# Performance work log

Measured on AMD Instinct MI355X. Metric: run time of the kernel, lower is better.

## Reference

```python
import jax, jax.numpy as jnp
import numpy as np

EPS = 1e-8       # slot-attention eps
LN_EPS = 1e-5    # torch LayerNorm default
ITERS = 3        # num_iterations


def _ln(x, g, b):
    m = jnp.mean(x, axis=-1, keepdims=True)
    v = jnp.var(x, axis=-1, keepdims=True)
    return (x - m) * jax.lax.rsqrt(v + LN_EPS) * g + b


def setup_inputs() -> dict:
    key = jax.random.key(0)
    ks = jax.random.split(key, 16)
    B, N, S, D = 64, 4096, 8, 256
    s = 1.0 / np.sqrt(D)
    inp = {}
    inp["inputs"] = jax.random.normal(ks[0], (B, N, D), jnp.float32)
    inp["init_slots"] = jax.random.normal(ks[1], (B, S, D), jnp.float32)
    inp["wq"] = jax.random.normal(ks[2], (D, D), jnp.float32) * s
    inp["bq"] = jnp.zeros((D,), jnp.float32)
    inp["wk"] = jax.random.normal(ks[3], (D, D), jnp.float32) * s
    inp["bk"] = jnp.zeros((D,), jnp.float32)
    inp["wv"] = jax.random.normal(ks[4], (D, D), jnp.float32) * s
    inp["bv"] = jnp.zeros((D,), jnp.float32)
    inp["w_ih"] = jax.random.normal(ks[5], (3 * D, D), jnp.float32) * s
    inp["b_ih"] = jnp.zeros((3 * D,), jnp.float32)
    inp["w_hh"] = jax.random.normal(ks[6], (3 * D, D), jnp.float32) * s
    inp["b_hh"] = jnp.zeros((3 * D,), jnp.float32)
    inp["w1"] = jax.random.normal(ks[7], (D, D), jnp.float32) * s  # fc1_slot (hidden_dim == D)
    inp["b1"] = jnp.zeros((D,), jnp.float32)
    inp["w2"] = jax.random.normal(ks[8], (D, D), jnp.float32) * s  # fc2_slot
    inp["b2"] = jnp.zeros((D,), jnp.float32)
    inp["g_in"] = jnp.ones((D,), jnp.float32)
    inp["b_in"] = jnp.zeros((D,), jnp.float32)
    inp["g_slots"] = jnp.ones((D,), jnp.float32)
    inp["b_slots"] = jnp.zeros((D,), jnp.float32)
    inp["g_ff"] = jnp.ones((D,), jnp.float32)
    inp["b_ff"] = jnp.zeros((D,), jnp.float32)
    return inp


def reference(inputs, init_slots, wq, bq, wk, bk, wv, bv, w_ih, b_ih, w_hh, b_hh,
              w1, b1, w2, b2, g_in, b_in, g_slots, b_slots, g_ff, b_ff):
    D = inputs.shape[-1]
    scale = D ** (-0.5)
    # img_k_v: LayerNorm inputs, project to k, v
    x = _ln(inputs, g_in, b_in)
    k = x @ wk.T + bk  # [B,N,D]
    v = x @ wv.T + bv  # [B,N,D]
    slots = init_slots  # [B,S,D]
    for _ in range(ITERS):
        prev = slots
        sn = _ln(slots, g_slots, b_slots)
        q = sn @ wq.T + bq                                   # [B,S,D]
        dots = jnp.einsum('bid,bjd->bij', q, k) * scale      # [B,S,N]
        attn = jax.nn.softmax(dots, axis=1) + EPS            # softmax over slots
        attn = attn / jnp.sum(attn, axis=-1, keepdims=True)  # normalize over inputs
        updates = jnp.einsum('bjd,bij->bid', v, attn)        # [B,S,D]
        # GRUCell(updates, prev): torch gate ordering r, z, n
        gx = updates @ w_ih.T + b_ih
        gh = prev @ w_hh.T + b_hh
        xr, xz, xn = jnp.split(gx, 3, axis=-1)
        hr, hz, hn = jnp.split(gh, 3, axis=-1)
        r = jax.nn.sigmoid(xr + hr)
        z = jax.nn.sigmoid(xz + hz)
        n = jnp.tanh(xn + r * hn)
        slots = (1.0 - z) * n + z * prev
        # residual MLP
        h = jax.nn.relu(_ln(slots, g_ff, b_ff) @ w1.T + b1)
        slots = slots + h @ w2.T + b2
    return slots
```

## Files before the change

### kernel.cpp

```cpp
#include <hip/hip_runtime.h>
#include <hip/hip_bf16.h>
#include <stdint.h>

typedef unsigned short u16;
typedef __attribute__((ext_vector_type(8))) short short8;
typedef __attribute__((ext_vector_type(4))) float f32x4;

#define NB 64
#define NN 4096
#define NS 8
#define ND 256
#define NSEG 16
#define GROWS (NB*NN)

__device__ inline u16 f2bf(float f) {
    uint32_t u = __float_as_uint(f);
    u = (u + 0x7FFFu + ((u >> 16) & 1u)) >> 16;
    return (u16)u;
}
__device__ inline float bf2f(u16 h) {
    return __uint_as_float(((uint32_t)h) << 16);
}
__device__ inline f32x4 mfma16(short8 a, short8 b, f32x4 c) {
    return __builtin_amdgcn_mfma_f32_16x16x32_bf16(a, b, c, 0, 0, 0);
}

__global__ __launch_bounds__(256) void prep_w(
        const float* __restrict__ wv, const float* __restrict__ wk, const float* __restrict__ wq,
        const float* __restrict__ wih, const float* __restrict__ whh,
        const float* __restrict__ w1, const float* __restrict__ w2,
        u16* __restrict__ wvb, u16* __restrict__ wkTb, u16* __restrict__ wqTb,
        u16* __restrict__ wihb, u16* __restrict__ whhb,
        u16* __restrict__ w1b, u16* __restrict__ w2b) {
    int i = blockIdx.x * 256 + threadIdx.x;
    if (i < 65536) { wvb[i] = f2bf(wv[i]); return; }
    i -= 65536;
    if (i < 65536) { wkTb[i] = f2bf(wk[(i & 255)*256 + (i >> 8)]); return; }
    i -= 65536;
    if (i < 65536) { wqTb[i] = f2bf(wq[(i & 255)*256 + (i >> 8)]); return; }
    i -= 65536;
    if (i < 196608) { wihb[i] = f2bf(wih[i]); return; }
    i -= 196608;
    if (i < 196608) { whhb[i] = f2bf(whh[i]); return; }
    i -= 196608;
    if (i < 65536) { w1b[i] = f2bf(w1[i]); return; }
    i -= 65536;
    if (i < 65536) w2b[i] = f2bf(w2[i]);
}

__global__ __launch_bounds__(256) void prep_M(
        const u16* __restrict__ wkTb, const u16* __restrict__ wqTb, u16* __restrict__ Mb,
        const float* __restrict__ wq, const float* __restrict__ bk, float* __restrict__ uvec) {
    if (blockIdx.x == 16) {
        int m = threadIdx.x;
        float acc = 0.f;
        for (int o = 0; o < 256; o++) acc += wq[o*256 + m] * bk[o];
        uvec[m] = acc;
        return;
    }
    const int d0 = blockIdx.x * 16;
    const int tid = threadIdx.x, wid = tid >> 6, lane = tid & 63;
    const int l15 = lane & 15, quad = lane >> 4, kq = quad * 8;
    short8 af[8];
#pragma unroll
    for (int k = 0; k < 8; k++)
        af[k] = *reinterpret_cast<const short8*>(&wkTb[(size_t)(d0 + l15)*256 + k*32 + kq]);
#pragma unroll
    for (int ct = 0; ct < 4; ct++) {
        int m0 = (wid*4 + ct)*16;
        f32x4 a = (f32x4){0.f,0.f,0.f,0.f};
#pragma unroll
        for (int k = 0; k < 8; k++) {
            short8 bw = *reinterpret_cast<const short8*>(&wqTb[(size_t)(m0 + l15)*256 + k*32 + kq]);
            a = mfma16(af[k], bw, a);
        }
#pragma unroll
        for (int r = 0; r < 4; r++)
            Mb[(size_t)(d0 + quad*4 + r)*256 + m0 + l15] = f2bf(a[r]);
    }
}

__global__ __launch_bounds__(256) void ln_cast(
        const float* __restrict__ inp, const float* __restrict__ g,
        const float* __restrict__ bt, u16* __restrict__ xb, u16* __restrict__ xT) {
    __shared__ u16 xs[64*268];
    const int tid = threadIdx.x, wid = tid >> 6, lane = tid & 63;
    const long r0 = (long)blockIdx.x * 64;
    const int rb = wid * 16;
    float4 g4 = reinterpret_cast<const float4*>(g)[lane];
    float4 b4 = reinterpret_cast<const float4*>(bt)[lane];
#pragma unroll 4
    for (int i = 0; i < 16; i++) {
        int row = rb + i;
        float4 v = reinterpret_cast<const float4*>(inp + (r0 + row)*256)[lane];
        float s = v.x + v.y + v.z + v.w;
        float ss = v.x*v.x + v.y*v.y + v.z*v.z + v.w*v.w;
#pragma unroll
        for (int off = 32; off >= 1; off >>= 1) { s += __shfl_xor(s, off, 64); ss += __shfl_xor(ss, off, 64); }
        float mean = s * (1.0f/256.0f);
        float rstd = rsqrtf(ss * (1.0f/256.0f) - mean*mean + 1e-5f);
        ushort4 o;
        o.x = f2bf((v.x-mean)*rstd*g4.x + b4.x);
        o.y = f2bf((v.y-mean)*rstd*g4.y + b4.y);
        o.z = f2bf((v.z-mean)*rstd*g4.z + b4.z);
        o.w = f2bf((v.w-mean)*rstd*g4.w + b4.w);
        reinterpret_cast<ushort4*>(xb + (r0 + row)*256)[lane] = o;
        int colb = (lane*4) ^ (((row >> 3) & 7) << 4);
        *reinterpret_cast<ushort4*>(&xs[row*268 + colb]) = o;
    }
    __syncthreads();
    const long bb = r0 >> 12, nb0 = r0 & 4095;
#pragma unroll
    for (int pass = 0; pass < 8; pass++) {
        const int d = pass*32 + wid*8 + (lane >> 3);
        const int nc = (lane & 7) * 8;
        const int colr = d ^ ((lane & 7) << 4);
        short8 val;
#pragma unroll
        for (int s2 = 0; s2 < 8; s2++)
            val[s2] = (short)xs[(nc + s2)*268 + colr];
        *reinterpret_cast<short8*>(&xT[((size_t)bb*256 + d)*4096 + nb0 + nc]) = val;
    }
}

__global__ __launch_bounds__(256) void q_proj(
        const float* __restrict__ slots, const u16* __restrict__ Mb,
        const float* __restrict__ uvec,
        const float* __restrict__ gs, const float* __restrict__ bs,
        u16* __restrict__ qb, float* __restrict__ cvec) {
    __shared__ u16 sn[16*264];
    const int b = blockIdx.x;
    const int tid = threadIdx.x, wid = tid >> 6, lane = tid & 63;
    const int l15 = lane & 15, kq = (lane >> 4) * 8;
    for (int rr = wid; rr < 8; rr += 4) {
        float4 v = reinterpret_cast<const float4*>(slots + (size_t)(b*8 + rr)*256)[lane];
        float s = v.x + v.y + v.z + v.w;
        float ss = v.x*v.x + v.y*v.y + v.z*v.z + v.w*v.w;
#pragma unroll
        for (int off = 32; off >= 1; off >>= 1) { s += __shfl_xor(s, off, 64); ss += __shfl_xor(ss, off, 64); }
        float mean = s * (1.f/256.f);
        float rstd = rsqrtf(ss * (1.f/256.f) - mean*mean + 1e-5f);
        float4 g4 = reinterpret_cast<const float4*>(gs)[lane];
        float4 b4 = reinterpret_cast<const float4*>(bs)[lane];
        ushort4 o;
        o.x = f2bf((v.x-mean)*rstd*g4.x + b4.x);
        o.y = f2bf((v.y-mean)*rstd*g4.y + b4.y);
        o.z = f2bf((v.z-mean)*rstd*g4.z + b4.z);
        o.w = f2bf((v.w-mean)*rstd*g4.w + b4.w);
        *reinterpret_cast<ushort4*>(&sn[rr*264 + lane*4]) = o;
    }
    {
        ushort4 z = {0,0,0,0};
        for (int rr = 8 + wid; rr < 16; rr += 4)
            *reinterpret_cast<ushort4*>(&sn[rr*264 + lane*4]) = z;
    }
    __syncthreads();
    {
        int s = tid >> 5, l = tid & 31;
        float p = 0.f;
#pragma unroll
        for (int i = 0; i < 8; i++)
            p += bf2f(sn[s*264 + l*8 + i]) * uvec[l*8 + i];
#pragma unroll
        for (int off = 16; off >= 1; off >>= 1) p += __shfl_xor(p, off, 64);
        if (l == 0) cvec[b*8 + s] = p;
    }
    short8 af[8];
#pragma unroll
    for (int k = 0; k < 8; k++) af[k] = *reinterpret_cast<const short8*>(&sn[l15*264 + k*32 + kq]);
#pragma unroll
    for (int ct = 0; ct < 4; ct++) {
        int o0 = (wid*4 + ct)*16;
        f32x4 a = (f32x4){0.f,0.f,0.f,0.f};
#pragma unroll
        for (int k = 0; k < 8; k++) {
            short8 bw = *reinterpret_cast<const short8*>(&Mb[(size_t)(o0 + l15)*256 + k*32 + kq]);
            a = mfma16(af[k], bw, a);
        }
        if (lane < 32) {
            int sb = (lane >> 4)*4;
#pragma unroll
            for (int r = 0; r < 4; r++)
                qb[(size_t)(b*8 + sb + r)*256 + o0 + l15] = f2bf(a[r]);
        }
    }
}

__global__ __launch_bounds__(256) void attn(
        const u16* __restrict__ qt, const u16* __restrict__ xrow,
        const u16* __restrict__ xcol, const float* __restrict__ cvec,
        float* __restrict__ num_part, float* __restrict__ den_part) {
    __shared__ u16 pb_all[4][16*72];
    __shared__ float red[4][8][260];
    __shared__ float redd[4][8];
    const int b = blockIdx.x >> 4;
    const int seg = blockIdx.x & 15;
    const int tid = threadIdx.x, wid = tid >> 6, lane = tid & 63;
    const int l15 = lane & 15, quad = lane >> 4, kq = quad * 8;
    u16* pb = pb_all[wid];
    {
        short8 z = {0,0,0,0,0,0,0,0};
        int r8 = 8 + (lane >> 3), c8 = (lane & 7)*8;
        *reinterpret_cast<short8*>(&pb[r8*72 + c8]) = z;
    }
    short8 aq[8];
    {
        const u16* qrow = &qt[((size_t)b*8 + (l15 & 7))*256 + kq];
        short8 z = {0,0,0,0,0,0,0,0};
#pragma unroll
        for (int kk = 0; kk < 8; kk++) {
            short8 t = *reinterpret_cast<const short8*>(&qrow[kk*32]);
            aq[kk] = (l15 < 8) ? t : z;
        }
    }
    float cc[4];
#pragma unroll
    for (int r = 0; r < 4; r++) {
        int rowi = quad*4 + r;
        cc[r] = (rowi < 8) ? cvec[b*8 + rowi] : 0.f;
    }
    const int n_w = seg*256 + wid*64;
    const u16* kbase = &xrow[((size_t)b*4096 + n_w + l15)*256 + kq];
    const u16* vbase = &xcol[((size_t)b*256 + l15)*4096 + n_w + kq];
    f32x4 acc[16];
#pragma unroll
    for (int dt = 0; dt < 16; dt++) acc[dt] = (f32x4){0.f,0.f,0.f,0.f};
    float psum[4] = {0.f,0.f,0.f,0.f};
    short8 kf[8];
#pragma unroll
    for (int kk = 0; kk < 8; kk++) kf[kk] = *reinterpret_cast<const short8*>(&kbase[kk*32]);

    f32x4 dots[4];
#pragma unroll
    for (int nt = 0; nt < 4; nt++) {
        short8 kn[8];
        if (nt < 3) {
            const u16* kp = kbase + (size_t)((nt+1)*16)*256;
#pragma unroll
            for (int kk = 0; kk < 8; kk++) kn[kk] = *reinterpret_cast<const short8*>(&kp[kk*32]);
        }
        f32x4 d = (f32x4){0.f,0.f,0.f,0.f};
#pragma unroll
        for (int kk = 0; kk < 8; kk++) d = mfma16(aq[kk], kf[kk], d);
        dots[nt] = d;
        if (nt < 3) {
#pragma unroll
            for (int kk = 0; kk < 8; kk++) kf[kk] = kn[kk];
        }
    }
    short8 v0[2], v1[2];
    {
        v0[0] = *reinterpret_cast<const short8*>(vbase);
        v1[0] = *reinterpret_cast<const short8*>(vbase + 32);
        const u16* vr2 = vbase + (size_t)16*4096;
        v0[1] = *reinterpret_cast<const short8*>(vr2);
        v1[1] = *reinterpret_cast<const short8*>(vr2 + 32);
    }
#pragma unroll
    for (int nt = 0; nt < 4; nt++) {
        float t0 = (dots[nt][0] + cc[0])*0.0625f, t1 = (dots[nt][1] + cc[1])*0.0625f;
        float t2 = (dots[nt][2] + cc[2])*0.0625f, t3 = (dots[nt][3] + cc[3])*0.0625f;
        float m4 = fmaxf(fmaxf(t0,t1), fmaxf(t2,t3));
        float m8 = fmaxf(m4, __shfl_xor(m4, 16, 64));
        float e0 = __expf(t0-m8), e1 = __expf(t1-m8), e2 = __expf(t2-m8), e3 = __expf(t3-m8);
        float s4 = e0+e1+e2+e3;
        float s8 = s4 + __shfl_xor(s4, 16, 64);
        float inv = 1.0f / s8;
        u16 h0 = f2bf(e0*inv + 1e-8f);
        u16 h1 = f2bf(e1*inv + 1e-8f);
        u16 h2 = f2bf(e2*inv + 1e-8f);
        u16 h3 = f2bf(e3*inv + 1e-8f);
        if (lane < 32) {
            int sb = quad*4, col = nt*16 + l15;
            pb[(sb+0)*72 + col] = h0;
            pb[(sb+1)*72 + col] = h1;
            pb[(sb+2)*72 + col] = h2;
            pb[(sb+3)*72 + col] = h3;
            psum[0] += bf2f(h0); psum[1] += bf2f(h1);
            psum[2] += bf2f(h2); psum[3] += bf2f(h3);
        }
    }
    __builtin_amdgcn_s_waitcnt(0xC07F);
    short8 ap0 = *reinterpret_cast<const short8*>(&pb[l15*72 + kq]);
    short8 ap1 = *reinterpret_cast<const short8*>(&pb[l15*72 + 32 + kq]);
#pragma unroll
    for (int dt = 0; dt < 16; dt++) {
        short8 nv0, nv1;
        if (dt < 14) {
            const u16* vn = vbase + (size_t)((dt+2)*16)*4096;
            nv0 = *reinterpret_cast<const short8*>(vn);
            nv1 = *reinterpret_cast<const short8*>(vn + 32);
        }
        acc[dt] = mfma16(ap0, v0[dt&1], acc[dt]);
        acc[dt] = mfma16(ap1, v1[dt&1], acc[dt]);
        if (dt < 14) { v0[dt&1] = nv0; v1[dt&1] = nv1; }
    }
#pragma unroll
    for (int off = 1; off < 16; off <<= 1) {
#pragma unroll
        for (int r = 0; r < 4; r++) psum[r] += __shfl_xor(psum[r], off, 64);
    }
    if (lane < 32) {
        int sb = quad*4;
#pragma unroll
        for (int dt = 0; dt < 16; dt++) {
            int d0 = dt*16 + l15;
#pragma unroll
            for (int r = 0; r < 4; r++)
                red[wid][sb+r][d0] = acc[dt][r];
        }
        if (l15 == 0) {
#pragma unroll
            for (int r = 0; r < 4; r++) redd[wid][sb+r] = psum[r];
        }
    }
    __syncthreads();
    for (int idx = tid; idx < 2048; idx += 256) {
        int s = idx >> 8, d = idx & 255;
        float v = red[0][s][d] + red[1][s][d] + red[2][s][d] + red[3][s][d];
        num_part[((size_t)(b*16 + seg)*8 + s)*256 + d] = v;
    }
    if (tid < 8)
        den_part[(b*16 + seg)*8 + tid] = redd[0][tid] + redd[1][tid] + redd[2][tid] + redd[3][tid];
}

__global__ __launch_bounds__(768) void finalize(
        const float* __restrict__ slots_in, const float* __restrict__ num_part, const float* __restrict__ den_part,
        const u16* __restrict__ wihb, const float* __restrict__ bih,
        const u16* __restrict__ whhb, const float* __restrict__ bhh,
        const u16* __restrict__ w1b, const float* __restrict__ b1v,
        const u16* __restrict__ w2b, const float* __restrict__ b2v,
        const u16* __restrict__ wvb, const float* __restrict__ bvv,
        const float* __restrict__ gff, const float* __restrict__ bff,
        float* __restrict__ slots_out,
        const u16* __restrict__ Mb, const float* __restrict__ uvec,
        const float* __restrict__ gs, const float* __restrict__ bs,
        u16* __restrict__ qb, float* __restrict__ cvec, int do_q) {
    __shared__ u16 updb[16*264];
    __shared__ u16 prevb[16*264];
    __shared__ u16 lnb[16*264];
    __shared__ float gx[8*776];
    __shared__ float gh[8*776];
    __shared__ float snew[8*256];
    __shared__ float dsum_s[8];
    float* sfin = gx;
    const int b = blockIdx.x;
    const int tid = threadIdx.x, wid = tid >> 6, lane = tid & 63;
    const int l15 = lane & 15, kq = (lane >> 4) * 8;
    if (tid < 8) {
        float ds = 0.f;
#pragma unroll
        for (int sg = 0; sg < 16; sg++) ds += den_part[(b*16 + sg)*8 + tid];
        dsum_s[tid] = ds;
    }
    __syncthreads();
    for (int idx = tid; idx < 2048; idx += 768) {
        int s = idx >> 8, d = idx & 255;
        float ns = 0.f;
#pragma unroll
        for (int sg = 0; sg < 16; sg++)
            ns += num_part[((size_t)(b*16 + sg)*8 + s)*256 + d];
        updb[s*264 + d] = f2bf(ns / dsum_s[s]);
        prevb[s*264 + d] = f2bf(slots_in[(size_t)(b*8 + s)*256 + d]);
        updb[(8+s)*264 + d] = 0;
        prevb[(8+s)*264 + d] = 0;
        lnb[(8+s)*264 + d] = 0;
    }
    __syncthreads();
    {
        short8 av[8];
#pragma unroll
        for (int k = 0; k < 8; k++)
            av[k] = *reinterpret_cast<const short8*>(&updb[l15*264 + k*32 + kq]);
        for (int ct = wid; ct < 16; ct += 12) {
            int o0 = ct*16;
            f32x4 a = (f32x4){0.f,0.f,0.f,0.f};
#pragma unroll
            for (int k = 0; k < 8; k++) {
                short8 bw = *reinterpret_cast<const short8*>(&wvb[(size_t)(o0 + l15)*256 + k*32 + kq]);
                a = mfma16(av[k], bw, a);
            }
            if (lane < 32) {
                int sb = (lane >> 4)*4, o = o0 + l15;
                float bb2 = bvv[o];
#pragma unroll
                for (int r = 0; r < 4; r++)
                    lnb[(sb+r)*264 + o] = f2bf(a[r] + bb2);
            }
        }
    }
    __syncthreads();
    short8 au[8], ap[8];
#pragma unroll
    for (int k = 0; k < 8; k++) {
        au[k] = *reinterpret_cast<const short8*>(&lnb[l15*264 + k*32 + kq]);
        ap[k] = *reinterpret_cast<const short8*>(&prevb[l15*264 + k*32 + kq]);
    }
#pragma unroll
    for (int ct = 0; ct < 4; ct++) {
        int o0 = (wid*4 + ct)*16;
        f32x4 ax = (f32x4){0.f,0.f,0.f,0.f}, ah = (f32x4){0.f,0.f,0.f,0.f};
#pragma unroll
        for (int k = 0; k < 8; k++) {
            short8 bx = *reinterpret_cast<const short8*>(&wihb[(size_t)(o0 + l15)*256 + k*32 + kq]);
            short8 bh = *reinterpret_cast<const short8*>(&whhb[(size_t)(o0 + l15)*256 + k*32 + kq]);
            ax = mfma16(au[k], bx, ax);
            ah = mfma16(ap[k], bh, ah);
        }
        if (lane < 32) {
            int sb = (lane >> 4)*4, o = o0 + l15;
            float bxs = bih[o], bhs = bhh[o];
#pragma unroll
            for (int r = 0; r < 4; r++) {
                gx[(sb+r)*776 + o] = ax[r] + bxs;
                gh[(sb+r)*776 + o] = ah[r] + bhs;
            }
        }
    }
    __syncthreads();
    for (int idx = tid; idx < 2048; idx += 768) {
        int s = idx >> 8, j = idx & 255;
        float xr = gx[s*776 + j], xz = gx[s*776 + 256 + j], xn = gx[s*776 + 512 + j];
        float hr = gh[s*776 + j], hz = gh[s*776 + 256 + j], hn = gh[s*776 + 512 + j];
        float r_ = 1.f/(1.f + __expf(-(xr+hr)));
        float z_ = 1.f/(1.f + __expf(-(xz+hz)));
        float n_ = tanhf(xn + r_*hn);
        float pv = slots_in[(size_t)(b*8 + s)*256 + j];
        snew[s*256 + j] = (1.f - z_)*n_ + z_*pv;
    }
    __syncthreads();
    if (wid < 8) {
        int rr = wid;
        float4 v = reinterpret_cast<const float4*>(&snew[rr*256])[lane];
        float s = v.x + v.y + v.z + v.w;
        float ss = v.x*v.x + v.y*v.y + v.z*v.z + v.w*v.w;
#pragma unroll
        for (int off = 32; off >= 1; off >>= 1) { s += __shfl_xor(s, off, 64); ss += __shfl_xor(ss, off, 64); }
        float mean = s * (1.f/256.f);
        float rstd = rsqrtf(ss * (1.f/256.f) - mean*mean + 1e-5f);
        float4 g4 = reinterpret_cast<const float4*>(gff)[lane];
        float4 b4 = reinterpret_cast<const float4*>(bff)[lane];
        ushort4 o;
        o.x = f2bf((v.x-mean)*rstd*g4.x + b4.x);
        o.y = f2bf((v.y-mean)*rstd*g4.y + b4.y);
        o.z = f2bf((v.z-mean)*rstd*g4.z + b4.z);
        o.w = f2bf((v.w-mean)*rstd*g4.w + b4.w);
        *reinterpret_cast<ushort4*>(&lnb[rr*264 + lane*4]) = o;
    } else {
        ushort4 z = {0,0,0,0};
        *reinterpret_cast<ushort4*>(&lnb[wid*264 + lane*4]) = z;
        *reinterpret_cast<ushort4*>(&lnb[(wid+4)*264 + lane*4]) = z;
    }
    __syncthreads();
    short8 al[8];
#pragma unroll
    for (int k = 0; k < 8; k++) al[k] = *reinterpret_cast<const short8*>(&lnb[l15*264 + k*32 + kq]);
    for (int ct = wid; ct < 16; ct += 12) {
        int o0 = ct*16;
        f32x4 a = (f32x4){0.f,0.f,0.f,0.f};
#pragma unroll
        for (int k = 0; k < 8; k++) {
            short8 bw = *reinterpret_cast<const short8*>(&w1b[(size_t)(o0 + l15)*256 + k*32 + kq]);
            a = mfma16(al[k], bw, a);
        }
        if (lane < 32) {
            int sb = (lane >> 4)*4, o = o0 + l15;
            float bb = b1v[o];
#pragma unroll
            for (int r = 0; r < 4; r++)
                updb[(sb+r)*264 + o] = f2bf(fmaxf(a[r] + bb, 0.f));
        }
    }
    __syncthreads();
    short8 ah2[8];
#pragma unroll
    for (int k = 0; k < 8; k++) ah2[k] = *reinterpret_cast<const short8*>(&updb[l15*264 + k*32 + kq]);
    for (int ct = wid; ct < 16; ct += 12) {
        int o0 = ct*16;
        f32x4 a = (f32x4){0.f,0.f,0.f,0.f};
#pragma unroll
        for (int k = 0; k < 8; k++) {
            short8 bw = *reinterpret_cast<const short8*>(&w2b[(size_t)(o0 + l15)*256 + k*32 + kq]);
            a = mfma16(ah2[k], bw, a);
        }
        if (lane < 32) {
            int sb = (lane >> 4)*4, o = o0 + l15;
            float bb = b2v[o];
#pragma unroll
            for (int r = 0; r < 4; r++) {
                float vfin = snew[(sb+r)*256 + o] + a[r] + bb;
                slots_out[(size_t)(b*8 + sb + r)*256 + o] = vfin;
                sfin[(sb+r)*256 + o] = vfin;
            }
        }
    }
    if (!do_q) return;
    __syncthreads();
    if (wid < 8) {
        int rr = wid;
        float4 v = reinterpret_cast<const float4*>(&sfin[rr*256])[lane];
        float s = v.x + v.y + v.z + v.w;
        float ss = v.x*v.x + v.y*v.y + v.z*v.z + v.w*v.w;
#pragma unroll
        for (int off = 32; off >= 1; off >>= 1) { s += __shfl_xor(s, off, 64); ss += __shfl_xor(ss, off, 64); }
        float mean = s * (1.f/256.f);
        float rstd = rsqrtf(ss * (1.f/256.f) - mean*mean + 1e-5f);
        float4 g4 = reinterpret_cast<const float4*>(gs)[lane];
        float4 b4 = reinterpret_cast<const float4*>(bs)[lane];
        ushort4 o;
        o.x = f2bf((v.x-mean)*rstd*g4.x + b4.x);
        o.y = f2bf((v.y-mean)*rstd*g4.y + b4.y);
        o.z = f2bf((v.z-mean)*rstd*g4.z + b4.z);
        o.w = f2bf((v.w-mean)*rstd*g4.w + b4.w);
        *reinterpret_cast<ushort4*>(&lnb[rr*264 + lane*4]) = o;
    } else {
        ushort4 z = {0,0,0,0};
        *reinterpret_cast<ushort4*>(&lnb[wid*264 + lane*4]) = z;
        *reinterpret_cast<ushort4*>(&lnb[(wid+4)*264 + lane*4]) = z;
    }
    __syncthreads();
    if (tid < 256) {
        int s = tid >> 5, l = tid & 31;
        float p = 0.f;
#pragma unroll
        for (int i = 0; i < 8; i++)
            p += bf2f(lnb[s*264 + l*8 + i]) * uvec[l*8 + i];
#pragma unroll
        for (int off = 16; off >= 1; off >>= 1) p += __shfl_xor(p, off, 64);
        if (l == 0) cvec[b*8 + s] = p;
    }
    short8 alq[8];
#pragma unroll
    for (int k = 0; k < 8; k++) alq[k] = *reinterpret_cast<const short8*>(&lnb[l15*264 + k*32 + kq]);
    for (int ct = wid; ct < 16; ct += 12) {
        int o0 = ct*16;
        f32x4 a = (f32x4){0.f,0.f,0.f,0.f};
#pragma unroll
        for (int k = 0; k < 8; k++) {
            short8 bw = *reinterpret_cast<const short8*>(&Mb[(size_t)(o0 + l15)*256 + k*32 + kq]);
            a = mfma16(alq[k], bw, a);
        }
        if (lane < 32) {
            int sb = (lane >> 4)*4, o = o0 + l15;
#pragma unroll
            for (int r = 0; r < 4; r++)
                qb[(size_t)(b*8 + sb + r)*256 + o] = f2bf(a[r]);
        }
    }
}

extern "C" void kernel_launch(void* const* d_in, const int* in_sizes, int n_in,
                              void* d_out, int out_size, void* d_ws, size_t ws_size,
                              hipStream_t stream) {
    (void)in_sizes; (void)n_in; (void)out_size;
    const float* inputs     = (const float*)d_in[0];
    const float* init_slots = (const float*)d_in[1];
    const float* wq  = (const float*)d_in[2];
    const float* bq  = (const float*)d_in[3];  (void)bq;
    const float* wk  = (const float*)d_in[4];
    const float* bk  = (const float*)d_in[5];
    const float* wv  = (const float*)d_in[6];
    const float* bv  = (const float*)d_in[7];
    const float* wih = (const float*)d_in[8];
    const float* bih = (const float*)d_in[9];
    const float* whh = (const float*)d_in[10];
    const float* bhh = (const float*)d_in[11];
    const float* w1  = (const float*)d_in[12];
    const float* b1  = (const float*)d_in[13];
    const float* w2  = (const float*)d_in[14];
    const float* b2  = (const float*)d_in[15];
    const float* g_in = (const float*)d_in[16];
    const float* b_in = (const float*)d_in[17];
    const float* g_sl = (const float*)d_in[18];
    const float* b_sl = (const float*)d_in[19];
    const float* g_ff = (const float*)d_in[20];
    const float* b_ff = (const float*)d_in[21];

    char* ws = (char*)d_ws;
    size_t off = 0;
    auto alloc = [&](size_t bytes) -> void* {
        void* p = ws + off;
        off += (bytes + 255) & ~(size_t)255;
        return p;
    };
    u16* xb    = (u16*)alloc((size_t)GROWS * ND * 2);
    u16* xT    = (u16*)alloc((size_t)GROWS * ND * 2);
    u16* qbf   = (u16*)alloc((size_t)NB * NS * ND * 2);
    float* slots = (float*)alloc((size_t)NB * NS * ND * 4);
    float* nump  = (float*)alloc((size_t)NB * NSEG * NS * ND * 4);
    float* denp  = (float*)alloc((size_t)NB * NSEG * NS * 4);
    float* cvec  = (float*)alloc((size_t)NB * NS * 4);
    float* uvec  = (float*)alloc(256 * 4);
    u16* wvb  = (u16*)alloc(65536 * 2);
    u16* wkTb = (u16*)alloc(65536 * 2);
    u16* wqTb = (u16*)alloc(65536 * 2);
    u16* Mb   = (u16*)alloc(65536 * 2);
    u16* wihb = (u16*)alloc(196608 * 2);
    u16* whhb = (u16*)alloc(196608 * 2);
    u16* w1b  = (u16*)alloc(65536 * 2);
    u16* w2b  = (u16*)alloc(65536 * 2);
    if (off > ws_size) return;

    prep_w<<<2816, 256, 0, stream>>>(wv, wk, wq, wih, whh, w1, w2,
                                     wvb, wkTb, wqTb, wihb, whhb, w1b, w2b);
    prep_M<<<17, 256, 0, stream>>>(wkTb, wqTb, Mb, wq, bk, uvec);
    hipMemcpyAsync(slots, init_slots, (size_t)NB * NS * ND * 4,
                   hipMemcpyDeviceToDevice, stream);
    ln_cast<<<GROWS / 64, 256, 0, stream>>>(inputs, g_in, b_in, xb, xT);
    q_proj<<<NB, 256, 0, stream>>>(slots, Mb, uvec, g_sl, b_sl, qbf, cvec);
    for (int it = 0; it < 3; it++) {
        attn<<<NB * 16, 256, 0, stream>>>(qbf, xb, xT, cvec, nump, denp);
        float* outp = (it == 2) ? (float*)d_out : slots;
        finalize<<<NB, 768, 0, stream>>>(slots, nump, denp, wihb, bih, whhb, bhh,
                                         w1b, b1, w2b, b2, wvb, bv, g_ff, b_ff, outp,
                                         Mb, uvec, g_sl, b_sl, qbf, cvec, (it < 2) ? 1 : 0);
    }
}
```

Before: 744.4 us.

## Split attn PV accumulation into two halves to cut registers and LDS

```diff
diff --git a/kernel.cpp b/kernel.cpp
--- a/kernel.cpp
+++ b/kernel.cpp
@@ -186,12 +186,12 @@
     }
 }
 
-__global__ __launch_bounds__(256) void attn(
+__global__ __launch_bounds__(256, 4) void attn(
         const u16* __restrict__ qt, const u16* __restrict__ xrow,
         const u16* __restrict__ xcol, const float* __restrict__ cvec,
         float* __restrict__ num_part, float* __restrict__ den_part) {
     __shared__ u16 pb_all[4][16*72];
-    __shared__ float red[4][8][260];
+    __shared__ float red[4][8][132];
     __shared__ float redd[4][8];
     const int b = blockIdx.x >> 4;
     const int seg = blockIdx.x & 15;
@@ -222,44 +222,28 @@
     const int n_w = seg*256 + wid*64;
     const u16* kbase = &xrow[((size_t)b*4096 + n_w + l15)*256 + kq];
     const u16* vbase = &xcol[((size_t)b*256 + l15)*4096 + n_w + kq];
-    f32x4 acc[16];
-#pragma unroll
-    for (int dt = 0; dt < 16; dt++) acc[dt] = (f32x4){0.f,0.f,0.f,0.f};
     float psum[4] = {0.f,0.f,0.f,0.f};
+    short8 v0[2], v1[2];
+    v0[0] = *reinterpret_cast<const short8*>(vbase);
+    v1[0] = *reinterpret_cast<const short8*>(vbase + 32);
+    v0[1] = *reinterpret_cast<const short8*>(vbase + (size_t)16*4096);
+    v1[1] = *reinterpret_cast<const short8*>(vbase + (size_t)16*4096 + 32);
     short8 kf[8];
 #pragma unroll
     for (int kk = 0; kk < 8; kk++) kf[kk] = *reinterpret_cast<const short8*>(&kbase[kk*32]);
-
-    f32x4 dots[4];
 #pragma unroll
     for (int nt = 0; nt < 4; nt++) {
+        f32x4 dd = (f32x4){0.f,0.f,0.f,0.f};
+#pragma unroll
+        for (int kk = 0; kk < 8; kk++) dd = mfma16(aq[kk], kf[kk], dd);
         short8 kn[8];
         if (nt < 3) {
             const u16* kp = kbase + (size_t)((nt+1)*16)*256;
 #pragma unroll
             for (int kk = 0; kk < 8; kk++) kn[kk] = *reinterpret_cast<const short8*>(&kp[kk*32]);
         }
-        f32x4 d = (f32x4){0.f,0.f,0.f,0.f};
-#pragma unroll
-        for (int kk = 0; kk < 8; kk++) d = mfma16(aq[kk], kf[kk], d);
-        dots[nt] = d;
-        if (nt < 3) {
-#pragma unroll
-            for (int kk = 0; kk < 8; kk++) kf[kk] = kn[kk];
-        }
-    }
-    short8 v0[2], v1[2];
-    {
-        v0[0] = *reinterpret_cast<const short8*>(vbase);
-        v1[0] = *reinterpret_cast<const short8*>(vbase + 32);
-        const u16* vr2 = vbase + (size_t)16*4096;
-        v0[1] = *reinterpret_cast<const short8*>(vr2);
-        v1[1] = *reinterpret_cast<const short8*>(vr2 + 32);
-    }
-#pragma unroll
-    for (int nt = 0; nt < 4; nt++) {
-        float t0 = (dots[nt][0] + cc[0])*0.0625f, t1 = (dots[nt][1] + cc[1])*0.0625f;
-        float t2 = (dots[nt][2] + cc[2])*0.0625f, t3 = (dots[nt][3] + cc[3])*0.0625f;
+        float t0 = (dd[0] + cc[0])*0.0625f, t1 = (dd[1] + cc[1])*0.0625f;
+        float t2 = (dd[2] + cc[2])*0.0625f, t3 = (dd[3] + cc[3])*0.0625f;
         float m4 = fmaxf(fmaxf(t0,t1), fmaxf(t2,t3));
         float m8 = fmaxf(m4, __shfl_xor(m4, 16, 64));
         float e0 = __expf(t0-m8), e1 = __expf(t1-m8), e2 = __expf(t2-m8), e3 = __expf(t3-m8);
@@ -279,22 +263,33 @@
             psum[0] += bf2f(h0); psum[1] += bf2f(h1);
             psum[2] += bf2f(h2); psum[3] += bf2f(h3);
         }
+        if (nt < 3) {
+#pragma unroll
+            for (int kk = 0; kk < 8; kk++) kf[kk] = kn[kk];
+        }
     }
     __builtin_amdgcn_s_waitcnt(0xC07F);
     short8 ap0 = *reinterpret_cast<const short8*>(&pb[l15*72 + kq]);
     short8 ap1 = *reinterpret_cast<const short8*>(&pb[l15*72 + 32 + kq]);
-#pragma unroll
-    for (int dt = 0; dt < 16; dt++) {
+    f32x4 acc8[8];
+#pragma unroll
+    for (int dt = 0; dt < 8; dt++) acc8[dt] = (f32x4){0.f,0.f,0.f,0.f};
+#pragma unroll
+    for (int dt = 0; dt < 8; dt++) {
         short8 nv0, nv1;
-        if (dt < 14) {
+        if (dt < 6) {
             const u16* vn = vbase + (size_t)((dt+2)*16)*4096;
             nv0 = *reinterpret_cast<const short8*>(vn);
             nv1 = *reinterpret_cast<const short8*>(vn + 32);
         }
-        acc[dt] = mfma16(ap0, v0[dt&1], acc[dt]);
-        acc[dt] = mfma16(ap1, v1[dt&1], acc[dt]);
-        if (dt < 14) { v0[dt&1] = nv0; v1[dt&1] = nv1; }
-    }
+        acc8[dt] = mfma16(ap0, v0[dt&1], acc8[dt]);
+        acc8[dt] = mfma16(ap1, v1[dt&1], acc8[dt]);
+        if (dt < 6) { v0[dt&1] = nv0; v1[dt&1] = nv1; }
+    }
+    v0[0] = *reinterpret_cast<const short8*>(vbase + (size_t)(8*16)*4096);
+    v1[0] = *reinterpret_cast<const short8*>(vbase + (size_t)(8*16)*4096 + 32);
+    v0[1] = *reinterpret_cast<const short8*>(vbase + (size_t)(9*16)*4096);
+    v1[1] = *reinterpret_cast<const short8*>(vbase + (size_t)(9*16)*4096 + 32);
 #pragma unroll
     for (int off = 1; off < 16; off <<= 1) {
 #pragma unroll
@@ -303,11 +298,11 @@
     if (lane < 32) {
         int sb = quad*4;
 #pragma unroll
-        for (int dt = 0; dt < 16; dt++) {
+        for (int dt = 0; dt < 8; dt++) {
             int d0 = dt*16 + l15;
 #pragma unroll
             for (int r = 0; r < 4; r++)
-                red[wid][sb+r][d0] = acc[dt][r];
+                red[wid][sb+r][d0] = acc8[dt][r];
         }
         if (l15 == 0) {
 #pragma unroll
@@ -315,13 +310,44 @@
         }
     }
     __syncthreads();
-    for (int idx = tid; idx < 2048; idx += 256) {
-        int s = idx >> 8, d = idx & 255;
+    for (int idx = tid; idx < 1024; idx += 256) {
+        int s = idx >> 7, d = idx & 127;
         float v = red[0][s][d] + red[1][s][d] + red[2][s][d] + red[3][s][d];
         num_part[((size_t)(b*16 + seg)*8 + s)*256 + d] = v;
     }
     if (tid < 8)
         den_part[(b*16 + seg)*8 + tid] = redd[0][tid] + redd[1][tid] + redd[2][tid] + redd[3][tid];
+    __syncthreads();
+#pragma unroll
+    for (int dt = 0; dt < 8; dt++) acc8[dt] = (f32x4){0.f,0.f,0.f,0.f};
+#pragma unroll
+    for (int dt = 0; dt < 8; dt++) {
+        short8 nv0, nv1;
+        if (dt < 6) {
+            const u16* vn = vbase + (size_t)((dt+10)*16)*4096;
+            nv0 = *reinterpret_cast<const short8*>(vn);
+            nv1 = *reinterpret_cast<const short8*>(vn + 32);
+        }
+        acc8[dt] = mfma16(ap0, v0[dt&1], acc8[dt]);
+        acc8[dt] = mfma16(ap1, v1[dt&1], acc8[dt]);
+        if (dt < 6) { v0[dt&1] = nv0; v1[dt&1] = nv1; }
+    }
+    if (lane < 32) {
+        int sb = quad*4;
+#pragma unroll
+        for (int dt = 0; dt < 8; dt++) {
+            int d0 = dt*16 + l15;
+#pragma unroll
+            for (int r = 0; r < 4; r++)
+                red[wid][sb+r][d0] = acc8[dt][r];
+        }
+    }
+    __syncthreads();
+    for (int idx = tid; idx < 1024; idx += 256) {
+        int s = idx >> 7, d = idx & 127;
+        float v = red[0][s][d] + red[1][s][d] + red[2][s][d] + red[3][s][d];
+        num_part[((size_t)(b*16 + seg)*8 + s)*256 + 128 + d] = v;
+    }
 }
 
 __global__ __launch_bounds__(768) void finalize(
```

Result: no change. 738.9 us (-0.7%).

## Drop transposed input copy; stage rows into LDS via async loads for PV

Applied to the files above, without the earlier changes.

```diff
diff --git a/kernel.cpp b/kernel.cpp
--- a/kernel.cpp
+++ b/kernel.cpp
@@ -23,6 +23,12 @@
 }
 __device__ inline f32x4 mfma16(short8 a, short8 b, f32x4 c) {
     return __builtin_amdgcn_mfma_f32_16x16x32_bf16(a, b, c, 0, 0, 0);
+}
+__device__ inline void gload_lds16(const u16* g, u16* l) {
+    __builtin_amdgcn_global_load_lds(
+        (const __attribute__((address_space(1))) void*)g,
+        (__attribute__((address_space(3))) void*)l,
+        16, 0, 0);
 }
 
 __global__ __launch_bounds__(256) void prep_w(
@@ -82,17 +88,15 @@
 
 __global__ __launch_bounds__(256) void ln_cast(
         const float* __restrict__ inp, const float* __restrict__ g,
-        const float* __restrict__ bt, u16* __restrict__ xb, u16* __restrict__ xT) {
-    __shared__ u16 xs[64*268];
+        const float* __restrict__ bt, u16* __restrict__ xb) {
     const int tid = threadIdx.x, wid = tid >> 6, lane = tid & 63;
-    const long r0 = (long)blockIdx.x * 64;
-    const int rb = wid * 16;
+    const long r0 = (long)blockIdx.x * 64 + wid * 16;
     float4 g4 = reinterpret_cast<const float4*>(g)[lane];
     float4 b4 = reinterpret_cast<const float4*>(bt)[lane];
 #pragma unroll 4
     for (int i = 0; i < 16; i++) {
-        int row = rb + i;
-        float4 v = reinterpret_cast<const float4*>(inp + (r0 + row)*256)[lane];
+        long row = r0 + i;
+        float4 v = reinterpret_cast<const float4*>(inp + row*256)[lane];
         float s = v.x + v.y + v.z + v.w;
         float ss = v.x*v.x + v.y*v.y + v.z*v.z + v.w*v.w;
 #pragma unroll
@@ -104,22 +108,7 @@
         o.y = f2bf((v.y-mean)*rstd*g4.y + b4.y);
         o.z = f2bf((v.z-mean)*rstd*g4.z + b4.z);
         o.w = f2bf((v.w-mean)*rstd*g4.w + b4.w);
-        reinterpret_cast<ushort4*>(xb + (r0 + row)*256)[lane] = o;
-        int colb = (lane*4) ^ (((row >> 3) & 7) << 4);
-        *reinterpret_cast<ushort4*>(&xs[row*268 + colb]) = o;
-    }
-    __syncthreads();
-    const long bb = r0 >> 12, nb0 = r0 & 4095;
-#pragma unroll
-    for (int pass = 0; pass < 8; pass++) {
-        const int d = pass*32 + wid*8 + (lane >> 3);
-        const int nc = (lane & 7) * 8;
-        const int colr = d ^ ((lane & 7) << 4);
-        short8 val;
-#pragma unroll
-        for (int s2 = 0; s2 < 8; s2++)
-            val[s2] = (short)xs[(nc + s2)*268 + colr];
-        *reinterpret_cast<short8*>(&xT[((size_t)bb*256 + d)*4096 + nb0 + nc]) = val;
+        reinterpret_cast<ushort4*>(xb + row*256)[lane] = o;
     }
 }
 
@@ -188,21 +177,31 @@
 
 __global__ __launch_bounds__(256) void attn(
         const u16* __restrict__ qt, const u16* __restrict__ xrow,
-        const u16* __restrict__ xcol, const float* __restrict__ cvec,
+        const float* __restrict__ cvec,
         float* __restrict__ num_part, float* __restrict__ den_part) {
-    __shared__ u16 pb_all[4][16*72];
-    __shared__ float red[4][8][260];
-    __shared__ float redd[4][8];
+    __shared__ u16 xt[4][32*256];
+    __shared__ u16 pb_all[4][16*36];
+    __shared__ float dpd[4][8];
     const int b = blockIdx.x >> 4;
     const int seg = blockIdx.x & 15;
     const int tid = threadIdx.x, wid = tid >> 6, lane = tid & 63;
     const int l15 = lane & 15, quad = lane >> 4, kq = quad * 8;
+    u16* xw = xt[wid];
     u16* pb = pb_all[wid];
+    const int n_w = seg*256 + wid*64;
+
     {
-        short8 z = {0,0,0,0,0,0,0,0};
-        int r8 = 8 + (lane >> 3), c8 = (lane & 7)*8;
-        *reinterpret_cast<short8*>(&pb[r8*72 + c8]) = z;
-    }
+        const int half = lane >> 5, c = lane & 31;
+#pragma unroll
+        for (int i = 0; i < 16; i++) {
+            const int r = i*2 + half;
+            const int key = (r & 7) ^ ((r >> 3) << 1);
+            gload_lds16(xrow + (size_t)(b*4096 + n_w + r)*256 + (c ^ key)*8, &xw[i*2*256]);
+        }
+    }
+#pragma unroll
+    for (int k2 = 0; k2 < 9; k2++) pb[lane + k2*64] = 0;
+
     short8 aq[8];
     {
         const u16* qrow = &qt[((size_t)b*8 + (l15 & 7))*256 + kq];
@@ -219,87 +218,88 @@
         int rowi = quad*4 + r;
         cc[r] = (rowi < 8) ? cvec[b*8 + rowi] : 0.f;
     }
-    const int n_w = seg*256 + wid*64;
-    const u16* kbase = &xrow[((size_t)b*4096 + n_w + l15)*256 + kq];
-    const u16* vbase = &xcol[((size_t)b*256 + l15)*4096 + n_w + kq];
     f32x4 acc[16];
 #pragma unroll
     for (int dt = 0; dt < 16; dt++) acc[dt] = (f32x4){0.f,0.f,0.f,0.f};
     float psum[4] = {0.f,0.f,0.f,0.f};
-    short8 kf[8];
-#pragma unroll
-    for (int kk = 0; kk < 8; kk++) kf[kk] = *reinterpret_cast<const short8*>(&kbase[kk*32]);
-
-    f32x4 dots[4];
-#pragma unroll
-    for (int nt = 0; nt < 4; nt++) {
-        short8 kn[8];
-        if (nt < 3) {
-            const u16* kp = kbase + (size_t)((nt+1)*16)*256;
-#pragma unroll
-            for (int kk = 0; kk < 8; kk++) kn[kk] = *reinterpret_cast<const short8*>(&kp[kk*32]);
-        }
-        f32x4 d = (f32x4){0.f,0.f,0.f,0.f};
-#pragma unroll
-        for (int kk = 0; kk < 8; kk++) d = mfma16(aq[kk], kf[kk], d);
-        dots[nt] = d;
-        if (nt < 3) {
-#pragma unroll
-            for (int kk = 0; kk < 8; kk++) kf[kk] = kn[kk];
-        }
-    }
-    short8 v0[2], v1[2];
-    {
-        v0[0] = *reinterpret_cast<const short8*>(vbase);
-        v1[0] = *reinterpret_cast<const short8*>(vbase + 32);
-        const u16* vr2 = vbase + (size_t)16*4096;
-        v0[1] = *reinterpret_cast<const short8*>(vr2);
-        v1[1] = *reinterpret_cast<const short8*>(vr2 + 32);
-    }
-#pragma unroll
-    for (int nt = 0; nt < 4; nt++) {
-        float t0 = (dots[nt][0] + cc[0])*0.0625f, t1 = (dots[nt][1] + cc[1])*0.0625f;
-        float t2 = (dots[nt][2] + cc[2])*0.0625f, t3 = (dots[nt][3] + cc[3])*0.0625f;
-        float m4 = fmaxf(fmaxf(t0,t1), fmaxf(t2,t3));
-        float m8 = fmaxf(m4, __shfl_xor(m4, 16, 64));
-        float e0 = __expf(t0-m8), e1 = __expf(t1-m8), e2 = __expf(t2-m8), e3 = __expf(t3-m8);
-        float s4 = e0+e1+e2+e3;
-        float s8 = s4 + __shfl_xor(s4, 16, 64);
-        float inv = 1.0f / s8;
-        u16 h0 = f2bf(e0*inv + 1e-8f);
-        u16 h1 = f2bf(e1*inv + 1e-8f);
-        u16 h2 = f2bf(e2*inv + 1e-8f);
-        u16 h3 = f2bf(e3*inv + 1e-8f);
-        if (lane < 32) {
-            int sb = quad*4, col = nt*16 + l15;
-            pb[(sb+0)*72 + col] = h0;
-            pb[(sb+1)*72 + col] = h1;
-            pb[(sb+2)*72 + col] = h2;
-            pb[(sb+3)*72 + col] = h3;
-            psum[0] += bf2f(h0); psum[1] += bf2f(h1);
-            psum[2] += bf2f(h2); psum[3] += bf2f(h3);
-        }
-    }
-    __builtin_amdgcn_s_waitcnt(0xC07F);
-    short8 ap0 = *reinterpret_cast<const short8*>(&pb[l15*72 + kq]);
-    short8 ap1 = *reinterpret_cast<const short8*>(&pb[l15*72 + 32 + kq]);
-#pragma unroll
-    for (int dt = 0; dt < 16; dt++) {
-        short8 nv0, nv1;
-        if (dt < 14) {
-            const u16* vn = vbase + (size_t)((dt+2)*16)*4096;
-            nv0 = *reinterpret_cast<const short8*>(vn);
-            nv1 = *reinterpret_cast<const short8*>(vn + 32);
-        }
-        acc[dt] = mfma16(ap0, v0[dt&1], acc[dt]);
-        acc[dt] = mfma16(ap1, v1[dt&1], acc[dt]);
-        if (dt < 14) { v0[dt&1] = nv0; v1[dt&1] = nv1; }
+
+    for (int ch = 0; ch < 2; ch++) {
+        const int nc = n_w + ch*32;
+        const u16* kbase = &xrow[((size_t)b*4096 + nc + l15)*256 + kq];
+        short8 kf[8], kn[8];
+#pragma unroll
+        for (int kk = 0; kk < 8; kk++) kf[kk] = *reinterpret_cast<const short8*>(&kbase[kk*32]);
+#pragma unroll
+        for (int nt = 0; nt < 2; nt++) {
+            f32x4 dd = (f32x4){0.f,0.f,0.f,0.f};
+            if (nt == 0) {
+#pragma unroll
+                for (int kk = 0; kk < 8; kk++) dd = mfma16(aq[kk], kf[kk], dd);
+                const u16* kp = kbase + (size_t)16*256;
+#pragma unroll
+                for (int kk = 0; kk < 8; kk++) kn[kk] = *reinterpret_cast<const short8*>(&kp[kk*32]);
+            } else {
+#pragma unroll
+                for (int kk = 0; kk < 8; kk++) dd = mfma16(aq[kk], kn[kk], dd);
+            }
+            float t0 = (dd[0] + cc[0])*0.0625f, t1 = (dd[1] + cc[1])*0.0625f;
+            float t2 = (dd[2] + cc[2])*0.0625f, t3 = (dd[3] + cc[3])*0.0625f;
+            float m4 = fmaxf(fmaxf(t0,t1), fmaxf(t2,t3));
+            float m8 = fmaxf(m4, __shfl_xor(m4, 16, 64));
+            float e0 = __expf(t0-m8), e1 = __expf(t1-m8), e2 = __expf(t2-m8), e3 = __expf(t3-m8);
+            float s4 = e0+e1+e2+e3;
+            float s8 = s4 + __shfl_xor(s4, 16, 64);
+            float inv = 1.0f / s8;
+            u16 h0 = f2bf(e0*inv + 1e-8f);
+            u16 h1 = f2bf(e1*inv + 1e-8f);
+            u16 h2 = f2bf(e2*inv + 1e-8f);
+            u16 h3 = f2bf(e3*inv + 1e-8f);
+            if (lane < 32) {
+                int sb = quad*4, col = nt*16 + l15;
+                pb[(sb+0)*36 + col] = h0;
+                pb[(sb+1)*36 + col] = h1;
+                pb[(sb+2)*36 + col] = h2;
+                pb[(sb+3)*36 + col] = h3;
+                psum[0] += bf2f(h0); psum[1] += bf2f(h1);
+                psum[2] += bf2f(h2); psum[3] += bf2f(h3);
+            }
+        }
+        __builtin_amdgcn_s_waitcnt(0x0070);
+        __builtin_amdgcn_sched_barrier(0);
+        short8 ap = *reinterpret_cast<const short8*>(&pb[l15*36 + kq]);
+        const int d = l15;
+#pragma unroll
+        for (int dt = 0; dt < 16; dt++) {
+            const int dd2 = dt*16 + d;
+            const int d3 = dd2 >> 3, d7 = dd2 & 7;
+            const int rowb = quad*8*256 + d7;
+            const int c3 = d3 ^ (quad << 1);
+            short8 pv;
+#pragma unroll
+            for (int j = 0; j < 8; j++)
+                pv[j] = (short)xw[rowb + j*256 + ((c3 ^ j) << 3)];
+            acc[dt] = mfma16(ap, pv, acc[dt]);
+        }
+        if (ch == 0) {
+            const int half = lane >> 5, c = lane & 31;
+#pragma unroll
+            for (int i = 0; i < 16; i++) {
+                const int r = i*2 + half;
+                const int key = (r & 7) ^ ((r >> 3) << 1);
+                gload_lds16(xrow + (size_t)(b*4096 + n_w + 32 + r)*256 + (c ^ key)*8, &xw[i*2*256]);
+            }
+        }
     }
 #pragma unroll
     for (int off = 1; off < 16; off <<= 1) {
 #pragma unroll
         for (int r = 0; r < 4; r++) psum[r] += __shfl_xor(psum[r], off, 64);
     }
+    if (quad < 2 && l15 == 0) {
+#pragma unroll
+        for (int r = 0; r < 4; r++) dpd[wid][quad*4 + r] = psum[r];
+    }
+    float* rw = (float*)&xt[wid][0];
     if (lane < 32) {
         int sb = quad*4;
 #pragma unroll
@@ -307,21 +307,17 @@
             int d0 = dt*16 + l15;
 #pragma unroll
             for (int r = 0; r < 4; r++)
-                red[wid][sb+r][d0] = acc[dt][r];
-        }
-        if (l15 == 0) {
-#pragma unroll
-            for (int r = 0; r < 4; r++) redd[wid][sb+r] = psum[r];
-        }
-    }
-    __syncthreads();
+                rw[(sb+r)*256 + d0] = acc[dt][r];
+        }
+    }
+    __syncthreads();
+    const float* F = (const float*)&xt[0][0];
     for (int idx = tid; idx < 2048; idx += 256) {
-        int s = idx >> 8, d = idx & 255;
-        float v = red[0][s][d] + red[1][s][d] + red[2][s][d] + red[3][s][d];
-        num_part[((size_t)(b*16 + seg)*8 + s)*256 + d] = v;
+        float v = F[idx] + F[4096 + idx] + F[8192 + idx] + F[12288 + idx];
+        num_part[((size_t)(b*16 + seg))*2048 + idx] = v;
     }
     if (tid < 8)
-        den_part[(b*16 + seg)*8 + tid] = redd[0][tid] + redd[1][tid] + redd[2][tid] + redd[3][tid];
+        den_part[(b*16 + seg)*8 + tid] = dpd[0][tid] + dpd[1][tid] + dpd[2][tid] + dpd[3][tid];
 }
 
 __global__ __launch_bounds__(768) void finalize(
@@ -584,7 +580,6 @@
         return p;
     };
     u16* xb    = (u16*)alloc((size_t)GROWS * ND * 2);
-    u16* xT    = (u16*)alloc((size_t)GROWS * ND * 2);
     u16* qbf   = (u16*)alloc((size_t)NB * NS * ND * 2);
     float* slots = (float*)alloc((size_t)NB * NS * ND * 4);
     float* nump  = (float*)alloc((size_t)NB * NSEG * NS * ND * 4);
@@ -606,10 +601,10 @@
     prep_M<<<17, 256, 0, stream>>>(wkTb, wqTb, Mb, wq, bk, uvec);
     hipMemcpyAsync(slots, init_slots, (size_t)NB * NS * ND * 4,
                    hipMemcpyDeviceToDevice, stream);
-    ln_cast<<<GROWS / 64, 256, 0, stream>>>(inputs, g_in, b_in, xb, xT);
+    ln_cast<<<GROWS / 64, 256, 0, stream>>>(inputs, g_in, b_in, xb);
     q_proj<<<NB, 256, 0, stream>>>(slots, Mb, uvec, g_sl, b_sl, qbf, cvec);
     for (int it = 0; it < 3; it++) {
-        attn<<<NB * 16, 256, 0, stream>>>(qbf, xb, xT, cvec, nump, denp);
+        attn<<<NB * 16, 256, 0, stream>>>(qbf, xb, cvec, nump, denp);
         float* outp = (it == 2) ? (float*)d_out : slots;
         finalize<<<NB, 768, 0, stream>>>(slots, nump, denp, wihb, bih, whhb, bhh,
                                          w1b, b1, w2b, b2, wvb, bv, g_ff, b_ff, outp,
```

After: 719.4 us. 1.03x faster.
